# Performance work log

Measured on AMD Instinct MI355X. Metric: run time of the kernel, lower is better.

## Reference

```python
import jax, jax.numpy as jnp
import numpy as np
from jax import lax

NUM_CHANNELS = 4
CHANNEL_OVERLAP = 1
BETA = 0.5
DN = ('NHWC', 'HWIO', 'NHWC')


def _conv_same(x, k2d):
    # x: [B,H,W,1], k2d: [kh,kw] -> 1-filter conv, same padding, no bias
    k = k2d[:, :, None, None]  # HWIO
    return lax.conv_general_dilated(x, k, (1, 1), 'SAME', dimension_numbers=DN)


def setup_inputs() -> dict:
    key = jax.random.key(0)
    k1, k2 = jax.random.split(key)
    sources = jax.random.uniform(k1, (NUM_CHANNELS, 32, 512, 512, 1), dtype=jnp.float32)
    # 6 (source, neighbor) pairs * 2 kernels each (contribution + interaction)
    kernels = jax.random.uniform(k2, (12, 3, 3), dtype=jnp.float32)  # NonNeg constraint -> uniform
    return {'sources': sources, 'kernels': kernels}


def reference(sources, kernels):
    # sources: [C,B,H,W,1]; kernels: [2*num_pairs, kh, kw]
    inv_p = 1.0 / (1.0 + BETA)
    corrected = []
    kidx = 0
    for i in range(NUM_CHANNELS):
        src = sources[i]
        bleed = None
        for off in range(-CHANNEL_OVERLAP, CHANNEL_OVERLAP + 1):
            if off == 0:
                continue
            j = i + off
            if not (0 <= j < NUM_CHANNELS):
                continue
            nb = sources[j]
            # direct bleed-through contribution
            contrib = _conv_same(nb, kernels[kidx]); kidx += 1
            # interaction term: (nb^beta * src)^(1/(1+beta))
            inter_term = (nb ** BETA * src) ** inv_p
            inter = _conv_same(inter_term, kernels[kidx]); kidx += 1
            term = contrib + inter
            bleed = term if bleed is None else bleed + term
        corrected.append(src - bleed)
    return jnp.stack(corrected)  # [C,B,H,W,1]
```

## Files before the change

### kernel.cpp

```cpp
#include <hip/hip_runtime.h>
#include <math.h>


#define NCH  4
#define NIMG 32
#define HH   512
#define WW   512

#define TW   64
#define TH   16
#define HTW  72
#define HTH  18
#define NTASK (NCH * HTH)

#if __has_builtin(__builtin_amdgcn_exp2f)
#define EXP2(x) __builtin_amdgcn_exp2f(x)
#else
#define EXP2(x) exp2f(x)
#endif
#if __has_builtin(__builtin_amdgcn_logf)
#define LOG2(x) __builtin_amdgcn_logf(x)
#else
#define LOG2(x) __log2f(x)
#endif

__device__ __forceinline__ float cbrtfast(float v) {
    return EXP2(0.33333334f * LOG2(v));
}

__device__ __forceinline__ void load_row6(const float* __restrict__ row, float w[6]) {
    const float4 m = *(const float4*)(row + 4);
    w[0] = row[3];
    w[1] = m.x; w[2] = m.y; w[3] = m.z; w[4] = m.w;
    w[5] = row[8];
}

template<int KCX, int KIX, int KCY, int KIY, bool CAPY>
__device__ __forceinline__ void edge_conv(
    const float (*Sx)[HTW], const float (*Sy)[HTW],
    int ty, int tx4, const float* __restrict__ ker,
    float accX[4], float accY[4], float cx[4], float cy[4])
{
    #pragma unroll
    for (int r = 0; r < 3; ++r) {
        float ax[6], ay[6];
        load_row6(&Sx[ty + r][tx4], ax);
        load_row6(&Sy[ty + r][tx4], ay);
        if (r == 1) {
            #pragma unroll
            for (int q = 0; q < 4; ++q) cx[q] = ax[q + 1];
            if (CAPY) {
                #pragma unroll
                for (int q = 0; q < 4; ++q) cy[q] = ay[q + 1];
            }
        }
        float ay2[6];
        #pragma unroll
        for (int q = 0; q < 6; ++q) ay2[q] = ay[q] * ay[q];

        {
            float w[6], t[6];
            #pragma unroll
            for (int q = 0; q < 6; ++q) {
                w[q] = ay2[q] * ay[q];
                t[q] = (ax[q] * ax[q]) * ay[q];
            }
            #pragma unroll
            for (int q = 0; q < 4; ++q) {
                float s = accX[q];
                #pragma unroll
                for (int dx = 0; dx < 3; ++dx) {
                    s = fmaf(w[q + dx], ker[KCX * 9 + r * 3 + dx], s);
                    s = fmaf(t[q + dx], ker[KIX * 9 + r * 3 + dx], s);
                }
                accX[q] = s;
            }
        }
        {
            float w[6], t[6];
            #pragma unroll
            for (int q = 0; q < 6; ++q) {
                w[q] = (ax[q] * ax[q]) * ax[q];
                t[q] = ay2[q] * ax[q];
            }
            #pragma unroll
            for (int q = 0; q < 4; ++q) {
                float s = accY[q];
                #pragma unroll
                for (int dx = 0; dx < 3; ++dx) {
                    s = fmaf(w[q + dx], ker[KCY * 9 + r * 3 + dx], s);
                    s = fmaf(t[q + dx], ker[KIY * 9 + r * 3 + dx], s);
                }
                accY[q] = s;
            }
        }
    }
}

__device__ __forceinline__ void store_out(float* __restrict__ p,
                                          const float c[4], const float a[4]) {
    float4 o;
    o.x = c[0] * c[0] * c[0] - a[0];
    o.y = c[1] * c[1] * c[1] - a[1];
    o.z = c[2] * c[2] * c[2] - a[2];
    o.w = c[3] * c[3] * c[3] - a[3];
    *(float4*)p = o;
}

__global__ __launch_bounds__(256) void bleed_kernel(
    const float* __restrict__ src,
    const float* __restrict__ ker,
    float* __restrict__ out)
{
    __shared__ __align__(16) float sA[NCH][HTH][HTW];

    const int tid    = threadIdx.x;
    const int tx     = tid & 15;
    const int ty     = tid >> 4;
    const int tx4    = tx * 4;
    const int tile_x = blockIdx.x * TW;
    const int tile_y = blockIdx.y * TH;
    const int n      = blockIdx.z;

    const size_t plane = (size_t)HH * WW;

    {
        const int g = tid >> 4;
        const int L = tid & 15;
        float4 vv[5];
        float  hv[5];
        #pragma unroll
        for (int it = 0; it < 5; ++it) {
            const int t   = g + it * 16;
            const int c   = t / HTH;
            const int row = t - c * HTH;
            const int gy  = tile_y - 1 + row;
            float4 v = make_float4(0.f, 0.f, 0.f, 0.f);
            float  h = 0.f;
            if (t < NTASK && (unsigned)gy < HH) {
                const float* rp = src + ((size_t)c * NIMG + n) * plane
                                      + (size_t)gy * WW;
                v = *(const float4*)(rp + tile_x + 4 * L);
                if (L == 0 && tile_x > 0)       h = rp[tile_x - 1];
                if (L == 1 && tile_x + TW < WW) h = rp[tile_x + TW];
            }
            vv[it] = v;
            hv[it] = h;
        }
        #pragma unroll
        for (int it = 0; it < 5; ++it) {
            const int t   = g + it * 16;
            if (t < NTASK) {
                const int c   = t / HTH;
                const int row = t - c * HTH;
                float4 a;
                a.x = cbrtfast(vv[it].x);
                a.y = cbrtfast(vv[it].y);
                a.z = cbrtfast(vv[it].z);
                a.w = cbrtfast(vv[it].w);
                const float ah = cbrtfast(hv[it]);
                *(float4*)&sA[c][row][4 + 4 * L] = a;
                if (L == 0) sA[c][row][3]  = ah;
                if (L == 1) sA[c][row][68] = ah;
            }
        }
    }
    __syncthreads();

    const int gy  = tile_y + ty;
    const int gx0 = tile_x + tx4;
    float* outp = out + (size_t)n * plane + (size_t)gy * WW + gx0;
    const size_t cstride = (size_t)NIMG * plane;

    float accL[4] = {0.f, 0.f, 0.f, 0.f};
    float accH[4] = {0.f, 0.f, 0.f, 0.f};
    float cA[4], cB[4];

    edge_conv<0, 1, 2, 3, false>(sA[0], sA[1], ty, tx4, ker, accL, accH, cA, cB);
    store_out(outp, cA, accL);

    #pragma unroll
    for (int q = 0; q < 4; ++q) { accL[q] = accH[q]; accH[q] = 0.f; }

    edge_conv<4, 5, 6, 7, false>(sA[1], sA[2], ty, tx4, ker, accL, accH, cA, cB);
    store_out(outp + cstride, cA, accL);

    #pragma unroll
    for (int q = 0; q < 4; ++q) { accL[q] = accH[q]; accH[q] = 0.f; }

    edge_conv<8, 9, 10, 11, true>(sA[2], sA[3], ty, tx4, ker, accL, accH, cA, cB);
    store_out(outp + 2 * cstride, cA, accL);
    store_out(outp + 3 * cstride, cB, accH);
}

extern "C" void kernel_launch(void* const* d_in, const int* in_sizes, int n_in,
                              void* d_out, int out_size, void* d_ws, size_t ws_size,
                              hipStream_t stream) {
    const float* src = (const float*)d_in[0];
    const float* ker = (const float*)d_in[1];
    float* out = (float*)d_out;

    dim3 grid(WW / TW, HH / TH, NIMG);
    dim3 block(256);
    bleed_kernel<<<grid, block, 0, stream>>>(src, ker, out);
}
```

Baseline: 238.6 us.

## Process two images per block with prefetch and separate halo LDS array

Each block now handles two images: it issues the global loads for both images up front, so the second image's loads overlap the first image's convolution, and the grid's z dimension is halved. It also adds a padded side array holding each thread's left and right neighbour values, so the unaligned halo reads avoid LDS bank conflicts. Plain __syncthreads is replaced by a custom barrier that waits only on LDS traffic. The cost is higher register pressure from holding two staged loads, fewer blocks in flight, and extra LDS writes for the halo array.

```diff
diff --git a/kernel.cpp b/kernel.cpp
--- a/kernel.cpp
+++ b/kernel.cpp
@@ -10,6 +10,7 @@
 #define TW   64
 #define TH   16
 #define HTW  72
+#define HSW  33
 #define HTH  18
 #define NTASK (NCH * HTH)
 
@@ -24,28 +25,37 @@
 #define LOG2(x) __log2f(x)
 #endif
 
+#define BAR_LDS() do {                                          \
+    asm volatile("s_waitcnt lgkmcnt(0)" ::: "memory");          \
+    __builtin_amdgcn_s_barrier();                               \
+    asm volatile("" ::: "memory");                              \
+} while (0)
+
 __device__ __forceinline__ float cbrtfast(float v) {
     return EXP2(0.33333334f * LOG2(v));
 }
 
-__device__ __forceinline__ void load_row6(const float* __restrict__ row, float w[6]) {
+__device__ __forceinline__ void load_row6(const float* __restrict__ row,
+                                          const float* __restrict__ hrow,
+                                          int tx, float w[6]) {
     const float4 m = *(const float4*)(row + 4);
-    w[0] = row[3];
+    w[0] = hrow[tx];
     w[1] = m.x; w[2] = m.y; w[3] = m.z; w[4] = m.w;
-    w[5] = row[8];
+    w[5] = hrow[16 + tx];
 }
 
 template<int KCX, int KIX, int KCY, int KIY, bool CAPY>
 __device__ __forceinline__ void edge_conv(
     const float (*Sx)[HTW], const float (*Sy)[HTW],
-    int ty, int tx4, const float* __restrict__ ker,
+    const float (*Hx)[HSW], const float (*Hy)[HSW],
+    int ty, int tx, int tx4, const float* __restrict__ ker,
     float accX[4], float accY[4], float cx[4], float cy[4])
 {
     #pragma unroll
     for (int r = 0; r < 3; ++r) {
         float ax[6], ay[6];
-        load_row6(&Sx[ty + r][tx4], ax);
-        load_row6(&Sy[ty + r][tx4], ay);
+        load_row6(&Sx[ty + r][tx4], Hx[ty + r], tx, ax);
+        load_row6(&Sy[ty + r][tx4], Hy[ty + r], tx, ay);
         if (r == 1) {
             #pragma unroll
             for (int q = 0; q < 4; ++q) cx[q] = ax[q + 1];
@@ -107,90 +117,130 @@
     *(float4*)p = o;
 }
 
+struct Stage {
+    float4 vv[5];
+    float  hv[5];
+};
+
+__device__ __forceinline__ void stage_load(
+    const float* __restrict__ src, int n, int tile_x, int tile_y,
+    int g, int L, size_t plane, Stage& st)
+{
+    #pragma unroll
+    for (int it = 0; it < 5; ++it) {
+        const int t   = g + it * 16;
+        const int c   = t / HTH;
+        const int row = t - c * HTH;
+        const int gy  = tile_y - 1 + row;
+        float4 v = make_float4(0.f, 0.f, 0.f, 0.f);
+        float  h = 0.f;
+        if (t < NTASK && (unsigned)gy < HH) {
+            const float* rp = src + ((size_t)c * NIMG + n) * plane
+                                  + (size_t)gy * WW;
+            v = *(const float4*)(rp + tile_x + 4 * L);
+            if (L == 0 && tile_x > 0)       h = rp[tile_x - 1];
+            if (L == 1 && tile_x + TW < WW) h = rp[tile_x + TW];
+        }
+        st.vv[it] = v;
+        st.hv[it] = h;
+    }
+}
+
+__device__ __forceinline__ void stage_write(
+    float (*sA)[HTH][HTW], float (*sH)[HTH][HSW],
+    int g, int L, const Stage& st)
+{
+    #pragma unroll
+    for (int it = 0; it < 5; ++it) {
+        const int t = g + it * 16;
+        if (t < NTASK) {
+            const int c   = t / HTH;
+            const int row = t - c * HTH;
+            float4 a;
+            a.x = cbrtfast(st.vv[it].x);
+            a.y = cbrtfast(st.vv[it].y);
+            a.z = cbrtfast(st.vv[it].z);
+            a.w = cbrtfast(st.vv[it].w);
+            const float ah = cbrtfast(st.hv[it]);
+            *(float4*)&sA[c][row][4 + 4 * L] = a;
+            if (L <= 14) sH[c][row][L + 1]  = a.w;
+            if (L >= 1)  sH[c][row][15 + L] = a.x;
+            if (L == 0)  sH[c][row][0]      = ah;
+            if (L == 1)  sH[c][row][31]     = ah;
+        }
+    }
+}
+
+__device__ __forceinline__ void conv_image(
+    const float (*sA)[HTH][HTW], const float (*sH)[HTH][HSW],
+    int ty, int tx, int tx4, const float* __restrict__ ker,
+    float* __restrict__ outp, size_t cstride)
+{
+    float accL[4] = {0.f, 0.f, 0.f, 0.f};
+    float accH[4] = {0.f, 0.f, 0.f, 0.f};
+    float cA[4], cB[4];
+
+    edge_conv<0, 1, 2, 3, false>(sA[0], sA[1], sH[0], sH[1],
+                                 ty, tx, tx4, ker, accL, accH, cA, cB);
+    store_out(outp, cA, accL);
+
+    #pragma unroll
+    for (int q = 0; q < 4; ++q) { accL[q] = accH[q]; accH[q] = 0.f; }
+
+    edge_conv<4, 5, 6, 7, false>(sA[1], sA[2], sH[1], sH[2],
+                                 ty, tx, tx4, ker, accL, accH, cA, cB);
+    store_out(outp + cstride, cA, accL);
+
+    #pragma unroll
+    for (int q = 0; q < 4; ++q) { accL[q] = accH[q]; accH[q] = 0.f; }
+
+    edge_conv<8, 9, 10, 11, true>(sA[2], sA[3], sH[2], sH[3],
+                                  ty, tx, tx4, ker, accL, accH, cA, cB);
+    store_out(outp + 2 * cstride, cA, accL);
+    store_out(outp + 3 * cstride, cB, accH);
+}
+
 __global__ __launch_bounds__(256) void bleed_kernel(
     const float* __restrict__ src,
     const float* __restrict__ ker,
     float* __restrict__ out)
 {
     __shared__ __align__(16) float sA[NCH][HTH][HTW];
+    __shared__ __align__(16) float sH[NCH][HTH][HSW];
 
     const int tid    = threadIdx.x;
     const int tx     = tid & 15;
     const int ty     = tid >> 4;
     const int tx4    = tx * 4;
+    const int g      = tid >> 4;
+    const int L      = tid & 15;
     const int tile_x = blockIdx.x * TW;
     const int tile_y = blockIdx.y * TH;
-    const int n      = blockIdx.z;
-
-    const size_t plane = (size_t)HH * WW;
-
-    {
-        const int g = tid >> 4;
-        const int L = tid & 15;
-        float4 vv[5];
-        float  hv[5];
-        #pragma unroll
-        for (int it = 0; it < 5; ++it) {
-            const int t   = g + it * 16;
-            const int c   = t / HTH;
-            const int row = t - c * HTH;
-            const int gy  = tile_y - 1 + row;
-            float4 v = make_float4(0.f, 0.f, 0.f, 0.f);
-            float  h = 0.f;
-            if (t < NTASK && (unsigned)gy < HH) {
-                const float* rp = src + ((size_t)c * NIMG + n) * plane
-                                      + (size_t)gy * WW;
-                v = *(const float4*)(rp + tile_x + 4 * L);
-                if (L == 0 && tile_x > 0)       h = rp[tile_x - 1];
-                if (L == 1 && tile_x + TW < WW) h = rp[tile_x + TW];
-            }
-            vv[it] = v;
-            hv[it] = h;
-        }
-        #pragma unroll
-        for (int it = 0; it < 5; ++it) {
-            const int t   = g + it * 16;
-            if (t < NTASK) {
-                const int c   = t / HTH;
-                const int row = t - c * HTH;
-                float4 a;
-                a.x = cbrtfast(vv[it].x);
-                a.y = cbrtfast(vv[it].y);
-                a.z = cbrtfast(vv[it].z);
-                a.w = cbrtfast(vv[it].w);
-                const float ah = cbrtfast(hv[it]);
-                *(float4*)&sA[c][row][4 + 4 * L] = a;
-                if (L == 0) sA[c][row][3]  = ah;
-                if (L == 1) sA[c][row][68] = ah;
-            }
-        }
-    }
-    __syncthreads();
+    const int n0     = blockIdx.z * 2;
+
+    const size_t plane   = (size_t)HH * WW;
+    const size_t cstride = (size_t)NIMG * plane;
 
     const int gy  = tile_y + ty;
     const int gx0 = tile_x + tx4;
-    float* outp = out + (size_t)n * plane + (size_t)gy * WW + gx0;
-    const size_t cstride = (size_t)NIMG * plane;
-
-    float accL[4] = {0.f, 0.f, 0.f, 0.f};
-    float accH[4] = {0.f, 0.f, 0.f, 0.f};
-    float cA[4], cB[4];
-
-    edge_conv<0, 1, 2, 3, false>(sA[0], sA[1], ty, tx4, ker, accL, accH, cA, cB);
-    store_out(outp, cA, accL);
-
-    #pragma unroll
-    for (int q = 0; q < 4; ++q) { accL[q] = accH[q]; accH[q] = 0.f; }
-
-    edge_conv<4, 5, 6, 7, false>(sA[1], sA[2], ty, tx4, ker, accL, accH, cA, cB);
-    store_out(outp + cstride, cA, accL);
-
-    #pragma unroll
-    for (int q = 0; q < 4; ++q) { accL[q] = accH[q]; accH[q] = 0.f; }
-
-    edge_conv<8, 9, 10, 11, true>(sA[2], sA[3], ty, tx4, ker, accL, accH, cA, cB);
-    store_out(outp + 2 * cstride, cA, accL);
-    store_out(outp + 3 * cstride, cB, accH);
+    float* outp0 = out + (size_t)n0 * plane + (size_t)gy * WW + gx0;
+
+    Stage s0, s1;
+    stage_load(src, n0, tile_x, tile_y, g, L, plane, s0);
+    stage_load(src, n0 + 1, tile_x, tile_y, g, L, plane, s1);
+    stage_write(sA, sH, g, L, s0);
+
+    BAR_LDS();
+
+    conv_image(sA, sH, ty, tx, tx4, ker, outp0, cstride);
+
+    BAR_LDS();
+
+    stage_write(sA, sH, g, L, s1);
+
+    BAR_LDS();
+
+    conv_image(sA, sH, ty, tx, tx4, ker, outp0 + plane, cstride);
 }
 
 extern "C" void kernel_launch(void* const* d_in, const int* in_sizes, int n_in,
@@ -200,7 +250,7 @@
     const float* ker = (const float*)d_in[1];
     float* out = (float*)d_out;
 
-    dim3 grid(WW / TW, HH / TH, NIMG);
+    dim3 grid(WW / TW, HH / TH, NIMG / 2);
     dim3 block(256);
     bleed_kernel<<<grid, block, 0, stream>>>(src, ker, out);
 }
```

Measured after the change: 252.3 us. +5.7%, slower.
